# Kernel optimization log

Hardware: AMD Instinct MI355X
Metric: run time of the kernel (lower is better)

The kernel has to match this reference:

```python
import itertools
import jax, jax.numpy as jnp
import numpy as np

DIM = 192
HEADS = 6
KEY_DIM = DIM // HEADS  # 32; attn_ratio=1 so d == key_dim
WS = 7
H = W = 56
MLP_HIDDEN = int(DIM * 4.0)
BN_EPS = 1e-5
LN_EPS = 1e-5


def _bias_idxs(ws):
    points = list(itertools.product(range(ws), range(ws)))
    offs, idxs = {}, []
    for p1 in points:
        for p2 in points:
            o = (abs(p1[0] - p2[0]), abs(p1[1] - p2[1]))
            offs.setdefault(o, len(offs))
            idxs.append(offs[o])
    N = len(points)
    return np.asarray(idxs, np.int32).reshape(N, N), len(offs)

BIAS_IDXS, NUM_OFFSETS = _bias_idxs(WS)  # (49,49), 49 offsets


def _ln(x, g, b):
    m = jnp.mean(x, -1, keepdims=True)
    v = jnp.mean(jnp.square(x - m), -1, keepdims=True)
    return (x - m) * jax.lax.rsqrt(v + LN_EPS) * g + b


def setup_inputs() -> dict:
    key = jax.random.key(0)
    ks = jax.random.split(key, 16)
    s = lambda fan: 1.0 / np.sqrt(fan)
    qkv_out = HEADS * KEY_DIM * 3  # 576
    return {
        'x': jax.random.normal(ks[0], (32, H * W, DIM), jnp.float32),
        'norm1_g': jnp.ones((DIM,), jnp.float32),
        'norm1_b': jnp.zeros((DIM,), jnp.float32),
        'qkv_w': jax.random.normal(ks[1], (DIM, qkv_out), jnp.float32) * s(DIM),
        'qkv_b': jnp.zeros((qkv_out,), jnp.float32),
        'attn_bias': jax.random.normal(ks[2], (HEADS, NUM_OFFSETS), jnp.float32) * 0.02,
        'proj_w': jax.random.normal(ks[3], (HEADS * KEY_DIM, DIM), jnp.float32) * s(DIM),
        'proj_b': jnp.zeros((DIM,), jnp.float32),
        'conv_w': jax.random.normal(ks[4], (DIM, 1, 3, 3), jnp.float32) * s(9),
        'bn_g': jnp.ones((DIM,), jnp.float32),
        'bn_b': jnp.zeros((DIM,), jnp.float32),
        'bn_mean': jnp.zeros((DIM,), jnp.float32),
        'bn_var': jnp.ones((DIM,), jnp.float32),
        'norm2_g': jnp.ones((DIM,), jnp.float32),
        'norm2_b': jnp.zeros((DIM,), jnp.float32),
        'fc1_w': jax.random.normal(ks[5], (DIM, MLP_HIDDEN), jnp.float32) * s(DIM),
        'fc1_b': jnp.zeros((MLP_HIDDEN,), jnp.float32),
        'fc2_w': jax.random.normal(ks[6], (MLP_HIDDEN, DIM), jnp.float32) * s(MLP_HIDDEN),
        'fc2_b': jnp.zeros((DIM,), jnp.float32),
    }


def _attention(xw, norm1_g, norm1_b, qkv_w, qkv_b, attn_bias, proj_w, proj_b):
    # xw: [Bw, 49, C]
    Bw, N, C = xw.shape
    h = _ln(xw, norm1_g, norm1_b)
    qkv = (h @ qkv_w + qkv_b).reshape(Bw, N, HEADS, 3 * KEY_DIM)
    q, k, v = jnp.split(qkv, 3, axis=-1)  # each [Bw, N, H, Kd]
    scale = KEY_DIM ** -0.5
    bias = attn_bias[:, BIAS_IDXS]  # [H, 49, 49] gather from offset table
    attn = jnp.einsum('bnhd,bmhd->bhnm', q, k) * scale + bias[None]
    attn = jax.nn.softmax(attn, axis=-1)
    out = jnp.einsum('bhnm,bmhd->bnhd', attn, v).reshape(Bw, N, HEADS * KEY_DIM)
    return out @ proj_w + proj_b


def reference(x, norm1_g, norm1_b, qkv_w, qkv_b, attn_bias, proj_w, proj_b,
              conv_w, bn_g, bn_b, bn_mean, bn_var,
              norm2_g, norm2_b, fc1_w, fc1_b, fc2_w, fc2_b):
    B, L, C = x.shape
    nH, nW = H // WS, W // WS
    res = x
    # window partition (H,W divisible by window -> no padding)
    xw = x.reshape(B, nH, WS, nW, WS, C).transpose(0, 1, 3, 2, 4, 5)
    xw = xw.reshape(B * nH * nW, WS * WS, C)
    xw = _attention(xw, norm1_g, norm1_b, qkv_w, qkv_b, attn_bias, proj_w, proj_b)
    xw = xw.reshape(B, nH, nW, WS, WS, C).transpose(0, 1, 3, 2, 4, 5).reshape(B, L, C)
    x = res + xw
    # depthwise 3x3 conv + BN (inference form)
    xc = x.transpose(0, 2, 1).reshape(B, C, H, W)
    xc = jax.lax.conv_general_dilated(
        xc, conv_w, window_strides=(1, 1), padding=((1, 1), (1, 1)),
        dimension_numbers=('NCHW', 'OIHW', 'NCHW'), feature_group_count=C)
    inv = jax.lax.rsqrt(bn_var + BN_EPS)
    xc = (xc - bn_mean[None, :, None, None]) * (bn_g * inv)[None, :, None, None] + bn_b[None, :, None, None]
    x = xc.reshape(B, C, L).transpose(0, 2, 1)
    # MLP (pre-LN)
    h = _ln(x, norm2_g, norm2_b)
    h = jax.nn.gelu(h @ fc1_w + fc1_b, approximate=False)
    x = x + (h @ fc2_w + fc2_b)
    return x
```

## Files before the change

### kernel.cpp

```cpp
#include <hip/hip_runtime.h>

#define CDIM   192
#define NHEADS 6
#define KDIM   32
#define NTOK   49
#define NPIX   3136
#define NB     32
#define NWIN   2048
#define CHUNKW 512
#define NCHUNK 4
#define CHUNKM (CHUNKW*NTOK)
#define QKVN   576
#define HIDDEN 768
#define LN_EPS 1e-5f
#define BN_EPS 1e-5f
#define WSTR   28224
#define NTOKALL 100352

typedef __attribute__((ext_vector_type(8))) short bf16x8;
typedef __attribute__((ext_vector_type(4))) float f32x4;

__device__ __forceinline__ unsigned short f2bf(float f) {
    unsigned u = __float_as_uint(f);
    return (unsigned short)((u + 0x7FFFu + ((u >> 16) & 1u)) >> 16);
}
__device__ __forceinline__ float bf2f(unsigned short s) {
    return __uint_as_float(((unsigned)s) << 16);
}

__device__ __forceinline__ float fast_gelu(float x) {
    float ax = fabsf(x);
    float t  = __builtin_amdgcn_rcpf(fmaf(0.23164190f, ax, 1.0f));
    float p  = fmaf(t, 1.061405429f, -1.453152027f);
    p = fmaf(t, p, 1.421413741f);
    p = fmaf(t, p, -0.284496736f);
    p = fmaf(t, p, 0.254829592f);
    p = p * t;
    float e  = __expf(-0.5f * x * x);
    float q  = ax * p * e;
    return 0.5f * (x + ax - q);
}

__global__ void kw_swz(const float* __restrict__ W, unsigned short* __restrict__ o,
                       int K, int N) {
    int t = blockIdx.x * 256 + threadIdx.x;
    int lane = t & 63, sub = t >> 6;
    int ksub = K >> 5;
    int total = (N >> 4) * ksub;
    if (sub >= total) return;
    int nfr = sub / ksub, kk = sub - nfr * ksub;
    int n = nfr * 16 + (lane & 15);
    int kb = kk * 32 + (lane >> 4) * 8;
    unsigned p0 = (unsigned)f2bf(W[(size_t)(kb + 0) * N + n]) |
                  ((unsigned)f2bf(W[(size_t)(kb + 1) * N + n]) << 16);
    unsigned p1 = (unsigned)f2bf(W[(size_t)(kb + 2) * N + n]) |
                  ((unsigned)f2bf(W[(size_t)(kb + 3) * N + n]) << 16);
    unsigned p2 = (unsigned)f2bf(W[(size_t)(kb + 4) * N + n]) |
                  ((unsigned)f2bf(W[(size_t)(kb + 5) * N + n]) << 16);
    unsigned p3 = (unsigned)f2bf(W[(size_t)(kb + 6) * N + n]) |
                  ((unsigned)f2bf(W[(size_t)(kb + 7) * N + n]) << 16);
    uint4 v = {p0, p1, p2, p3};
    *(uint4*)(o + (size_t)(sub * 64 + lane) * 8) = v;
}

__global__ void k_prep_conv(const float* __restrict__ cw,
    const float* __restrict__ bg, const float* __restrict__ bb,
    const float* __restrict__ bm, const float* __restrict__ bv,
    float* __restrict__ cwT, float* __restrict__ bnsc, float* __restrict__ bnbi)
{
    int t = threadIdx.x + blockIdx.x * 256;
    if (t < 9 * CDIM) {
        int tap = t / CDIM, c = t - tap * CDIM;
        cwT[t] = cw[c * 9 + tap];
    }
    if (t < CDIM) {
        float s = bg[t] * rsqrtf(bv[t] + BN_EPS);
        bnsc[t] = s;
        bnbi[t] = bb[t] - bm[t] * s;
    }
}

__global__ void k0_stats(const float* __restrict__ x, float* __restrict__ mv) {
    int t    = blockIdx.x * 4 + (threadIdx.x >> 6);
    int lane = threadIdx.x & 63;
    const float* row = x + (size_t)t * CDIM;
    float e0 = row[lane], e1 = row[lane + 64], e2 = row[lane + 128];
    float s = e0 + e1 + e2;
    for (int o = 32; o; o >>= 1) s += __shfl_xor(s, o);
    float m = s * (1.0f / 192.0f);
    float d0 = e0 - m, d1 = e1 - m, d2 = e2 - m;
    float v = d0*d0 + d1*d1 + d2*d2;
    for (int o = 32; o; o >>= 1) v += __shfl_xor(v, o);
    if (lane == 0) {
        mv[t] = m;
        mv[NTOKALL + t] = 1.0f / sqrtf(v * (1.0f / 192.0f) + LN_EPS);
    }
}

__global__ __launch_bounds__(256) void k1_qkv_mfma(
    const float* __restrict__ x,  const float* __restrict__ mv,
    const float* __restrict__ g1, const float* __restrict__ b1,
    const unsigned short* __restrict__ wsw, const float* __restrict__ qb,
    unsigned short* __restrict__ qkv, int wbase)
{
    const int tid = threadIdx.x;
    const int w = tid >> 6, L = tid & 63, quad = L >> 4, l15 = L & 15;
    const int m0 = blockIdx.x * 64;
    const int Nt = blockIdx.y;
    int mA = m0 + w * 16 + l15;
    int gt = wbase * NTOK + mA;
    int wg = gt / 49, tok = gt - wg * 49;
    int bb = wg >> 6, wrem = wg & 63;
    int rr = tok / 7, cc = tok - rr * 7;
    int xrow = bb * NPIX + ((wrem >> 3) * 7 + rr) * 56 + (wrem & 7) * 7 + cc;
    float mean = mv[xrow], rstd = mv[NTOKALL + xrow];
    const float* xr = x + (size_t)xrow * CDIM;
    bf16x8 a[6];
#pragma unroll
    for (int kk = 0; kk < 6; ++kk) {
        int c0 = kk * 32 + quad * 8;
        float4 xv0 = *(const float4*)&xr[c0], xv1 = *(const float4*)&xr[c0 + 4];
        float4 gv0 = *(const float4*)&g1[c0], gv1 = *(const float4*)&g1[c0 + 4];
        float4 bv0 = *(const float4*)&b1[c0], bv1 = *(const float4*)&b1[c0 + 4];
        bf16x8 av;
        av[0] = (short)f2bf((xv0.x - mean) * rstd * gv0.x + bv0.x);
        av[1] = (short)f2bf((xv0.y - mean) * rstd * gv0.y + bv0.y);
        av[2] = (short)f2bf((xv0.z - mean) * rstd * gv0.z + bv0.z);
        av[3] = (short)f2bf((xv0.w - mean) * rstd * gv0.w + bv0.w);
        av[4] = (short)f2bf((xv1.x - mean) * rstd * gv1.x + bv1.x);
        av[5] = (short)f2bf((xv1.y - mean) * rstd * gv1.y + bv1.y);
        av[6] = (short)f2bf((xv1.z - mean) * rstd * gv1.z + bv1.z);
        av[7] = (short)f2bf((xv1.w - mean) * rstd * gv1.w + bv1.w);
        a[kk] = av;
    }
    f32x4 acc[12];
#pragma unroll
    for (int nf = 0; nf < 12; ++nf) acc[nf] = (f32x4){0.f, 0.f, 0.f, 0.f};
    const bf16x8* B = (const bf16x8*)wsw;
#pragma unroll
    for (int kk = 0; kk < 6; ++kk) {
#pragma unroll
        for (int nf = 0; nf < 12; ++nf) {
            bf16x8 bfr = B[(size_t)((Nt * 12 + nf) * 6 + kk) * 64 + L];
            acc[nf] = __builtin_amdgcn_mfma_f32_16x16x32_bf16(a[kk], bfr, acc[nf], 0, 0, 0);
        }
    }
    float qbv[12];
#pragma unroll
    for (int nf = 0; nf < 12; ++nf) qbv[nf] = qb[Nt * 192 + nf * 16 + l15];
#pragma unroll
    for (int i = 0; i < 4; ++i) {
        int mrow = m0 + w * 16 + quad * 4 + i;
        int wrel = mrow / 49, tokr = mrow - wrel * 49;
        unsigned short* obase = qkv + (size_t)wrel * WSTR + tokr * 32;
#pragma unroll
        for (int nf = 0; nf < 12; ++nf) {
            int n = Nt * 192 + nf * 16 + l15;
            int h = n / 96, rem = n - h * 96;
            int part = rem >> 5, d = rem & 31;
            obase[(size_t)(part * 6 + h) * 1568 + d] = f2bf(acc[nf][i] + qbv[nf]);
        }
    }
}

__global__ __launch_bounds__(128) void k2_attn(
    unsigned short* __restrict__ qkv, const float* __restrict__ abias)
{
    __shared__ float kv[6272];
    const int wrel = blockIdx.x / 3;
    const int pair = blockIdx.x - wrel * 3;
    const int h0 = pair * 2;
    unsigned short* base = qkv + (size_t)wrel * WSTR;
    for (int idx = threadIdx.x; idx < 784; idx += 128) {
        int part = idx / 392;
        int rem  = idx - part * 392;
        int h    = rem / 196;
        int off8 = rem - h * 196;
        bf16x8 v = *(const bf16x8*)&base[(size_t)((part + 1) * 6 + h0 + h) * 1568 + off8 * 8];
        float* dst = &kv[((part * 2 + h) * 196 + off8) * 8];
        float4 f0 = {bf2f((unsigned short)v[0]), bf2f((unsigned short)v[1]),
                     bf2f((unsigned short)v[2]), bf2f((unsigned short)v[3])};
        float4 f1 = {bf2f((unsigned short)v[4]), bf2f((unsigned short)v[5]),
                     bf2f((unsigned short)v[6]), bf2f((unsigned short)v[7])};
        *(float4*)&dst[0] = f0;
        *(float4*)&dst[4] = f1;
    }
    __syncthreads();
    const int item = threadIdx.x;
    if (item >= 98) return;
    const int h = item / 49;
    const int row = item - h * 49;
    const int hg = h0 + h;
    unsigned short* qptr = base + (size_t)hg * 1568 + row * 32;
    float4 q4[8];
#pragma unroll
    for (int dq2 = 0; dq2 < 4; ++dq2) {
        bf16x8 v = *(const bf16x8*)&qptr[dq2 * 8];
        q4[dq2 * 2]     = (float4){bf2f((unsigned short)v[0]), bf2f((unsigned short)v[1]),
                                   bf2f((unsigned short)v[2]), bf2f((unsigned short)v[3])};
        q4[dq2 * 2 + 1] = (float4){bf2f((unsigned short)v[4]), bf2f((unsigned short)v[5]),
                                   bf2f((unsigned short)v[6]), bf2f((unsigned short)v[7])};
    }
    const int rr = row / 7, rc = row - rr * 7;
    const float scale = 0.17677669529663687f;
    const float* kbase = &kv[(h * 49) * 32];
    const float* vbase = &kv[(98 + h * 49) * 32];
    float s[49];
    for (int j = 0; j < 49; ++j) {
        const float* kr = kbase + j * 32;
        float4 a = {0, 0, 0, 0};
#pragma unroll
        for (int dq = 0; dq < 8; ++dq) {
            float4 k4 = *(const float4*)&kr[dq * 4];
            a.x += q4[dq].x * k4.x; a.y += q4[dq].y * k4.y;
            a.z += q4[dq].z * k4.z; a.w += q4[dq].w * k4.w;
        }
        int jr = j / 7, jc = j - jr * 7;
        int dy = rr > jr ? rr - jr : jr - rr;
        int dx = rc > jc ? rc - jc : jc - rc;
        s[j] = (a.x + a.y + a.z + a.w) * scale + abias[hg * 49 + dy * 7 + dx];
    }
    float mx = s[0];
    for (int j = 1; j < 49; ++j) mx = fmaxf(mx, s[j]);
    float sum = 0.0f;
    for (int j = 0; j < 49; ++j) { s[j] = __expf(s[j] - mx); sum += s[j]; }
    float rinv = 1.0f / sum;
    float4 o[8] = {};
    for (int j = 0; j < 49; ++j) {
        float p = s[j];
        const float* vr = vbase + j * 32;
#pragma unroll
        for (int dq = 0; dq < 8; ++dq) {
            float4 v4 = *(const float4*)&vr[dq * 4];
            o[dq].x += p * v4.x; o[dq].y += p * v4.y;
            o[dq].z += p * v4.z; o[dq].w += p * v4.w;
        }
    }
#pragma unroll
    for (int dq = 0; dq < 8; ++dq) {
        uint2 pk;
        pk.x = (unsigned)f2bf(o[dq].x * rinv) | ((unsigned)f2bf(o[dq].y * rinv) << 16);
        pk.y = (unsigned)f2bf(o[dq].z * rinv) | ((unsigned)f2bf(o[dq].w * rinv) << 16);
        *(uint2*)&qptr[dq * 4] = pk;
    }
}

__global__ __launch_bounds__(256) void k3_proj_mfma(
    const unsigned short* __restrict__ qkv, const float* __restrict__ x,
    const unsigned short* __restrict__ wsw, const float* __restrict__ pb,
    float* __restrict__ x1, int wbase)
{
    const int tid = threadIdx.x;
    const int w = tid >> 6, L = tid & 63, quad = L >> 4, l15 = L & 15;
    const int m0 = blockIdx.x * 64;
    const int Nt = blockIdx.y;
    int mA = m0 + w * 16 + l15;
    int wrelA = mA / 49, tokA = mA - wrelA * 49;
    const unsigned short* ar = qkv + (size_t)wrelA * WSTR + tokA * 32 + quad * 8;
    bf16x8 a[6];
#pragma unroll
    for (int kk = 0; kk < 6; ++kk)
        a[kk] = *(const bf16x8*)&ar[(size_t)kk * 1568];
    f32x4 acc[4];
#pragma unroll
    for (int nf = 0; nf < 4; ++nf) acc[nf] = (f32x4){0.f, 0.f, 0.f, 0.f};
    const bf16x8* B = (const bf16x8*)wsw;
#pragma unroll
    for (int kk = 0; kk < 6; ++kk) {
#pragma unroll
        for (int nf = 0; nf < 4; ++nf) {
            bf16x8 bfr = B[(size_t)((Nt * 4 + nf) * 6 + kk) * 64 + L];
            acc[nf] = __builtin_amdgcn_mfma_f32_16x16x32_bf16(a[kk], bfr, acc[nf], 0, 0, 0);
        }
    }
    float pbv[4];
#pragma unroll
    for (int nf = 0; nf < 4; ++nf) pbv[nf] = pb[Nt * 64 + nf * 16 + l15];
#pragma unroll
    for (int i = 0; i < 4; ++i) {
        int mrow = m0 + w * 16 + quad * 4 + i;
        int wrel = mrow / 49, tokr = mrow - wrel * 49;
        int wg = wbase + wrel;
        int bb = wg >> 6, wrem = wg & 63;
        int r = tokr / 7, c = tokr - r * 7;
        size_t xoff = ((size_t)(bb * NPIX + ((wrem >> 3) * 7 + r) * 56 + (wrem & 7) * 7 + c)) * CDIM;
#pragma unroll
        for (int nf = 0; nf < 4; ++nf) {
            int col = Nt * 64 + nf * 16 + l15;
            x1[xoff + col] = acc[nf][i] + pbv[nf] + x[xoff + col];
        }
    }
}

__global__ __launch_bounds__(256) void k4_convln(
    const float* __restrict__ x1, const float* __restrict__ cwT,
    const float* __restrict__ bnsc, const float* __restrict__ bnbi,
    float* __restrict__ x2, float* __restrict__ mv)
{
    const int w = threadIdx.x >> 6, lane = threadIdx.x & 63;
    const int bid = blockIdx.x;
    const int sbid = (bid & 7) * 3136 + (bid >> 3);
    const int t = sbid * 4 + w;
    const int b = t / NPIX, l = t - b * NPIX;
    const int yy = l / 56, xx = l - yy * 56;
    const bool act = lane < 48;
    const int c0 = lane * 4;
    float4 o = {0, 0, 0, 0};
    if (act) {
        const float* xb = x1 + (size_t)b * NPIX * CDIM;
        float4 acc = {0, 0, 0, 0};
#pragma unroll
        for (int dy = -1; dy <= 1; ++dy) {
            int y2 = yy + dy;
            if ((unsigned)y2 >= 56u) continue;
#pragma unroll
            for (int dx = -1; dx <= 1; ++dx) {
                int x2c = xx + dx;
                if ((unsigned)x2c >= 56u) continue;
                float4 v = *(const float4*)&xb[(size_t)(y2 * 56 + x2c) * CDIM + c0];
                int tap = (dy + 1) * 3 + (dx + 1);
                float4 wt = *(const float4*)&cwT[tap * CDIM + c0];
                acc.x += v.x * wt.x;
                acc.y += v.y * wt.y;
                acc.z += v.z * wt.z;
                acc.w += v.w * wt.w;
            }
        }
        float4 sc = *(const float4*)&bnsc[c0];
        float4 bi = *(const float4*)&bnbi[c0];
        o.x = acc.x * sc.x + bi.x;
        o.y = acc.y * sc.y + bi.y;
        o.z = acc.z * sc.z + bi.z;
        o.w = acc.w * sc.w + bi.w;
        *(float4*)&x2[(size_t)t * CDIM + c0] = o;
    }
    float s = o.x + o.y + o.z + o.w;
    for (int off = 32; off; off >>= 1) s += __shfl_xor(s, off);
    float m = s * (1.0f / 192.0f);
    float d0 = o.x - m, d1 = o.y - m, d2 = o.z - m, d3 = o.w - m;
    float v2 = act ? (d0*d0 + d1*d1 + d2*d2 + d3*d3) : 0.0f;
    for (int off = 32; off; off >>= 1) v2 += __shfl_xor(v2, off);
    if (lane == 0) {
        mv[t] = m;
        mv[NTOKALL + t] = 1.0f / sqrtf(v2 * (1.0f / 192.0f) + LN_EPS);
    }
}

__global__ __launch_bounds__(256) void k5_mlp_mfma(
    const float* __restrict__ x2, const float* __restrict__ mv2,
    const float* __restrict__ g2, const float* __restrict__ b2,
    const unsigned short* __restrict__ w1sw, const float* __restrict__ fb1,
    const unsigned short* __restrict__ w2sw, const float* __restrict__ fb2,
    float* __restrict__ out)
{
    __shared__ unsigned short aFrag[24 * 512];
    __shared__ unsigned short hsw[16 * 512];
    const int tid = threadIdx.x;
    const int w = tid >> 6, L = tid & 63, quad = L >> 4, l15 = L & 15;
    const int m0 = blockIdx.x * 64;
#pragma unroll
    for (int rsl = 0; rsl < 6; ++rsl) {
        int s = tid + 256 * rsl;
        int mf = s / 384, rem = s - mf * 384;
        int kk = rem >> 6, La = rem & 63;
        int row = m0 + mf * 16 + (La & 15);
        int c0 = kk * 32 + (La >> 4) * 8;
        float mm = mv2[row], rs = mv2[NTOKALL + row];
        const float* xr = x2 + (size_t)row * CDIM + c0;
        float4 xv0 = *(const float4*)&xr[0], xv1 = *(const float4*)&xr[4];
        float4 gv0 = *(const float4*)&g2[c0], gv1 = *(const float4*)&g2[c0 + 4];
        float4 bv0 = *(const float4*)&b2[c0], bv1 = *(const float4*)&b2[c0 + 4];
        bf16x8 av;
        av[0] = (short)f2bf((xv0.x - mm) * rs * gv0.x + bv0.x);
        av[1] = (short)f2bf((xv0.y - mm) * rs * gv0.y + bv0.y);
        av[2] = (short)f2bf((xv0.z - mm) * rs * gv0.z + bv0.z);
        av[3] = (short)f2bf((xv0.w - mm) * rs * gv0.w + bv0.w);
        av[4] = (short)f2bf((xv1.x - mm) * rs * gv1.x + bv1.x);
        av[5] = (short)f2bf((xv1.y - mm) * rs * gv1.y + bv1.y);
        av[6] = (short)f2bf((xv1.z - mm) * rs * gv1.z + bv1.z);
        av[7] = (short)f2bf((xv1.w - mm) * rs * gv1.w + bv1.w);
        *(bf16x8*)&aFrag[(size_t)s * 8] = av;
    }
    __syncthreads();

    f32x4 acc2[4][3];
#pragma unroll
    for (int mf = 0; mf < 4; ++mf)
#pragma unroll
        for (int nf = 0; nf < 3; ++nf) acc2[mf][nf] = (f32x4){0.f, 0.f, 0.f, 0.f};
    const bf16x8* B1 = (const bf16x8*)w1sw;
    const bf16x8* B2 = (const bf16x8*)w2sw;

    for (int ch = 0; ch < 6; ++ch) {
        f32x4 acc1[4][2];
#pragma unroll
        for (int mf = 0; mf < 4; ++mf)
#pragma unroll
            for (int nf = 0; nf < 2; ++nf) acc1[mf][nf] = (f32x4){0.f, 0.f, 0.f, 0.f};
#pragma unroll
        for (int kk = 0; kk < 6; ++kk) {
            bf16x8 bfr0 = B1[(size_t)((ch * 8 + 2 * w + 0) * 6 + kk) * 64 + L];
            bf16x8 bfr1 = B1[(size_t)((ch * 8 + 2 * w + 1) * 6 + kk) * 64 + L];
#pragma unroll
            for (int mf = 0; mf < 4; ++mf) {
                bf16x8 av = *(const bf16x8*)&aFrag[(size_t)((mf * 6 + kk) * 64 + L) * 8];
                acc1[mf][0] = __builtin_amdgcn_mfma_f32_16x16x32_bf16(av, bfr0, acc1[mf][0], 0, 0, 0);
                acc1[mf][1] = __builtin_amdgcn_mfma_f32_16x16x32_bf16(av, bfr1, acc1[mf][1], 0, 0, 0);
            }
        }
        __syncthreads();
#pragma unroll
        for (int mf = 0; mf < 4; ++mf) {
#pragma unroll
            for (int nf = 0; nf < 2; ++nf) {
                float bias = fb1[ch * 128 + 32 * w + nf * 16 + l15];
                int hi16 = (((nf * 16 + l15) >> 3) & 3) << 4;
#pragma unroll
                for (int i = 0; i < 4; ++i) {
                    float h = acc1[mf][nf][i] + bias;
                    h = fast_gelu(h);
                    int Ls = (quad * 4 + i) | hi16;
                    hsw[(w * 4 + mf) * 512 + Ls * 8 + (L & 7)] = f2bf(h);
                }
            }
        }
        __syncthreads();
#pragma unroll
        for (int kk2 = 0; kk2 < 4; ++kk2) {
            bf16x8 a2[4];
#pragma unroll
            for (int mf = 0; mf < 4; ++mf)
                a2[mf] = *(const bf16x8*)&hsw[(size_t)((kk2 * 4 + mf) * 512) + (size_t)L * 8];
#pragma unroll
            for (int nf = 0; nf < 3; ++nf) {
                bf16x8 bfr = B2[(size_t)((w * 3 + nf) * 24 + ch * 4 + kk2) * 64 + L];
#pragma unroll
                for (int mf = 0; mf < 4; ++mf)
                    acc2[mf][nf] = __builtin_amdgcn_mfma_f32_16x16x32_bf16(a2[mf], bfr, acc2[mf][nf], 0, 0, 0);
            }
        }
    }
    float fb2v[3];
#pragma unroll
    for (int nf = 0; nf < 3; ++nf) fb2v[nf] = fb2[w * 48 + nf * 16 + l15];
#pragma unroll
    for (int mf = 0; mf < 4; ++mf) {
#pragma unroll
        for (int i = 0; i < 4; ++i) {
            int row = m0 + mf * 16 + quad * 4 + i;
            const float* xr = x2 + (size_t)row * CDIM;
            float* orow = out + (size_t)row * CDIM;
#pragma unroll
            for (int nf = 0; nf < 3; ++nf) {
                int col = w * 48 + nf * 16 + l15;
                orow[col] = acc2[mf][nf][i] + fb2v[nf] + xr[col];
            }
        }
    }
}

extern "C" void kernel_launch(void* const* d_in, const int* in_sizes, int n_in,
                              void* d_out, int out_size, void* d_ws, size_t ws_size,
                              hipStream_t stream) {
    const float* x     = (const float*)d_in[0];
    const float* g1    = (const float*)d_in[1];
    const float* b1    = (const float*)d_in[2];
    const float* qkvw  = (const float*)d_in[3];
    const float* qkvb  = (const float*)d_in[4];
    const float* abias = (const float*)d_in[5];
    const float* projw = (const float*)d_in[6];
    const float* projb = (const float*)d_in[7];
    const float* convw = (const float*)d_in[8];
    const float* bng   = (const float*)d_in[9];
    const float* bnb   = (const float*)d_in[10];
    const float* bnm   = (const float*)d_in[11];
    const float* bnv   = (const float*)d_in[12];
    const float* g2    = (const float*)d_in[13];
    const float* b2    = (const float*)d_in[14];
    const float* fc1w  = (const float*)d_in[15];
    const float* fc1b  = (const float*)d_in[16];
    const float* fc2w  = (const float*)d_in[17];
    const float* fc2b  = (const float*)d_in[18];
    float* out = (float*)d_out;

    float* wsf   = (float*)d_ws;
    unsigned short* qkvws = (unsigned short*)wsf;
    float* x2b   = wsf;
    float* mv    = wsf + 19267584;
    unsigned short* qkvw_sw = (unsigned short*)(wsf + 19468288);
    unsigned short* projw_sw = qkvw_sw + 110592;
    unsigned short* fc1_sw   = projw_sw + 36864;
    unsigned short* fc2_sw   = fc1_sw + 147456;
    float* cwT  = wsf + 19689472;
    float* bnsc = cwT + 1728;
    float* bnbi = bnsc + 192;

    kw_swz<<<(216 * 64 + 255) / 256, 256, 0, stream>>>(qkvw, qkvw_sw, CDIM, QKVN);
    kw_swz<<<(72  * 64 + 255) / 256, 256, 0, stream>>>(projw, projw_sw, CDIM, CDIM);
    kw_swz<<<(288 * 64 + 255) / 256, 256, 0, stream>>>(fc1w, fc1_sw, CDIM, HIDDEN);
    kw_swz<<<(288 * 64 + 255) / 256, 256, 0, stream>>>(fc2w, fc2_sw, HIDDEN, CDIM);
    k_prep_conv<<<7, 256, 0, stream>>>(convw, bng, bnb, bnm, bnv, cwT, bnsc, bnbi);

    k0_stats<<<NTOKALL / 4, 256, 0, stream>>>(x, mv);
    for (int chunk = 0; chunk < NCHUNK; ++chunk) {
        int wbase = chunk * CHUNKW;
        k1_qkv_mfma<<<dim3(CHUNKM / 64, 3), 256, 0, stream>>>(
            x, mv, g1, b1, qkvw_sw, qkvb, qkvws, wbase);
        k2_attn<<<CHUNKW * 3, 128, 0, stream>>>(qkvws, abias);
        k3_proj_mfma<<<dim3(CHUNKM / 64, 3), 256, 0, stream>>>(
            qkvws, x, projw_sw, projb, out, wbase);
    }
    k4_convln<<<NTOKALL / 4, 256, 0, stream>>>(out, cwT, bnsc, bnbi, x2b, mv);
    k5_mlp_mfma<<<NTOKALL / 64, 256, 0, stream>>>(
        x2b, mv, g2, b2, fc1_sw, fc1b, fc2_sw, fc2b, out);
}
```

Before: 852.4 us.

## Use fewer attention chunks based on workspace size and remap block order per XCD

Drops the four-chunk attention loop in favour of one or two chunks, chosen by whether the workspace can hold the full QKV buffer. Fewer chunks means fewer kernel launches and larger grids per launch. The QKV and projection kernels now use a flattened 1D grid whose block index is remapped so that consecutive blocks, spread across the 8 XCDs, work on neighbouring M tiles and share the N tiles of the same rows in cache. The workspace layout changes with the chunk choice, which adds a risk if ws_size is misjudged, and the remap assumes the grid is divisible by 8.

```diff
diff --git a/kernel.cpp b/kernel.cpp
--- a/kernel.cpp
+++ b/kernel.cpp
@@ -7,9 +7,6 @@
 #define NPIX   3136
 #define NB     32
 #define NWIN   2048
-#define CHUNKW 512
-#define NCHUNK 4
-#define CHUNKM (CHUNKW*NTOK)
 #define QKVN   576
 #define HIDDEN 768
 #define LN_EPS 1e-5f
@@ -105,8 +102,10 @@
 {
     const int tid = threadIdx.x;
     const int w = tid >> 6, L = tid & 63, quad = L >> 4, l15 = L & 15;
-    const int m0 = blockIdx.x * 64;
-    const int Nt = blockIdx.y;
+    const int nper = gridDim.x >> 3;
+    const int hh = (blockIdx.x & 7) * nper + (blockIdx.x >> 3);
+    const int m0 = (hh / 3) * 64;
+    const int Nt = hh % 3;
     int mA = m0 + w * 16 + l15;
     int gt = wbase * NTOK + mA;
     int wg = gt / 49, tok = gt - wg * 49;
@@ -252,8 +251,10 @@
 {
     const int tid = threadIdx.x;
     const int w = tid >> 6, L = tid & 63, quad = L >> 4, l15 = L & 15;
-    const int m0 = blockIdx.x * 64;
-    const int Nt = blockIdx.y;
+    const int nper = gridDim.x >> 3;
+    const int hh = (blockIdx.x & 7) * nper + (blockIdx.x >> 3);
+    const int m0 = (hh / 3) * 64;
+    const int Nt = hh % 3;
     int mA = m0 + w * 16 + l15;
     int wrelA = mA / 49, tokA = mA - wrelA * 49;
     const unsigned short* ar = qkv + (size_t)wrelA * WSTR + tokA * 32 + quad * 8;
@@ -483,17 +484,30 @@
     const float* fc2b  = (const float*)d_in[18];
     float* out = (float*)d_out;
 
-    float* wsf   = (float*)d_ws;
-    unsigned short* qkvws = (unsigned short*)wsf;
-    float* x2b   = wsf;
-    float* mv    = wsf + 19267584;
-    unsigned short* qkvw_sw = (unsigned short*)(wsf + 19468288);
+    float* wsf = (float*)d_ws;
+
+    const size_t needA = 29325376ull * 4;
+    int nchunk, chunkw;
+    float *mv, *cwT, *bnsc, *bnbi;
+    unsigned short *qkvw_sw;
+    if (ws_size >= needA) {
+        nchunk = 1;  chunkw = 2048;
+        mv      = wsf + 28901376;
+        qkvw_sw = (unsigned short*)(wsf + 29102080);
+        cwT     = wsf + 29323264;
+    } else {
+        nchunk = 2;  chunkw = 1024;
+        mv      = wsf + 19267584;
+        qkvw_sw = (unsigned short*)(wsf + 19468288);
+        cwT     = wsf + 19689472;
+    }
+    unsigned short* qkvws    = (unsigned short*)wsf;
+    float*          x2b      = wsf;
     unsigned short* projw_sw = qkvw_sw + 110592;
     unsigned short* fc1_sw   = projw_sw + 36864;
     unsigned short* fc2_sw   = fc1_sw + 147456;
-    float* cwT  = wsf + 19689472;
-    float* bnsc = cwT + 1728;
-    float* bnbi = bnsc + 192;
+    bnsc = cwT + 1728;
+    bnbi = bnsc + 192;
 
     kw_swz<<<(216 * 64 + 255) / 256, 256, 0, stream>>>(qkvw, qkvw_sw, CDIM, QKVN);
     kw_swz<<<(72  * 64 + 255) / 256, 256, 0, stream>>>(projw, projw_sw, CDIM, CDIM);
@@ -502,12 +516,13 @@
     k_prep_conv<<<7, 256, 0, stream>>>(convw, bng, bnb, bnm, bnv, cwT, bnsc, bnbi);
 
     k0_stats<<<NTOKALL / 4, 256, 0, stream>>>(x, mv);
-    for (int chunk = 0; chunk < NCHUNK; ++chunk) {
-        int wbase = chunk * CHUNKW;
-        k1_qkv_mfma<<<dim3(CHUNKM / 64, 3), 256, 0, stream>>>(
+    for (int chunk = 0; chunk < nchunk; ++chunk) {
+        int wbase = chunk * chunkw;
+        int mt = chunkw * NTOK / 64;
+        k1_qkv_mfma<<<mt * 3, 256, 0, stream>>>(
             x, mv, g1, b1, qkvw_sw, qkvb, qkvws, wbase);
-        k2_attn<<<CHUNKW * 3, 128, 0, stream>>>(qkvws, abias);
-        k3_proj_mfma<<<dim3(CHUNKM / 64, 3), 256, 0, stream>>>(
+        k2_attn<<<chunkw * 3, 128, 0, stream>>>(qkvws, abias);
+        k3_proj_mfma<<<mt * 3, 256, 0, stream>>>(
             qkvws, x, projw_sw, projb, out, wbase);
     }
     k4_convln<<<NTOKALL / 4, 256, 0, stream>>>(out, cwT, bnsc, bnbi, x2b, mv);
```

New measurement: 725.9 us. -14.8%, faster.
